# Kernel tuning notes

Hardware: AMD Instinct MI355X
Metric: run time of the kernel (lower is better)

## Reference

```python
import jax, jax.numpy as jnp
import numpy as np

DIM = 32          # image/vq dim (ImageTransform3D default dim=32 == vq.layers[0].dim)
CODEBOOK = 1024   # number of codebook entries
TOTAL = 4194304   # flat weight-vector length (multiple of DIM)


def setup_inputs() -> dict:
    key = jax.random.key(0)
    k1, k2, k3 = jax.random.split(key, 3)
    weights = jax.random.normal(k1, (TOTAL,), dtype=jnp.float32)
    condition = jax.random.normal(k2, (1, DIM, TOTAL // DIM), dtype=jnp.float32)
    codebook = jax.random.normal(k3, (CODEBOOK, DIM), dtype=jnp.float32)
    return {"weights": weights, "condition": condition, "codebook": codebook}


def reference(weights, condition, codebook):
    # --- ImageTransform3D.forward: pad flat weights to a multiple of DIM, view (1, DIM, -1)
    pad = (-weights.shape[0]) % DIM  # static
    if pad:
        weights = jnp.concatenate([weights, jnp.zeros((pad,), weights.dtype)])
    img = weights.reshape(1, DIM, -1)
    # --- TokenTransform3D: subtract condition, flatten to tokens of size DIM
    x = (img - condition).reshape(-1, DIM)  # [N, DIM]
    # --- VectorQuantize (freeze_codebook, eval): nearest-neighbour lookup
    d = (
        jnp.sum(x * x, axis=-1, keepdims=True)
        - 2.0 * (x @ codebook.T)
        + jnp.sum(codebook * codebook, axis=-1)
    )
    indices = jnp.argmin(d, axis=-1)  # [N] int32
    return indices
```

## Files before the change

kernel.cpp:

```cpp
#include <hip/hip_runtime.h>

#define TOTAL     4194304
#define DIM       32
#define NTOK      (TOTAL / DIM)
#define NCODE     1024
#define NCHUNK    8
#define CCODES    128
#define DELTA_EPS 2e-3f
#define FLAGBIT   0x40000000

typedef _Float16 half8   __attribute__((ext_vector_type(8)));
typedef float    floatx4 __attribute__((ext_vector_type(4)));

#define GLOAD_LDS16(g, l) \
    __builtin_amdgcn_global_load_lds((const __attribute__((address_space(1))) void*)(g), \
                                     (__attribute__((address_space(3))) void*)(l), 16, 0, 0)
#define GLOAD_LDS4(g, l) \
    __builtin_amdgcn_global_load_lds((const __attribute__((address_space(1))) void*)(g), \
                                     (__attribute__((address_space(3))) void*)(l), 4, 0, 0)

__global__ __launch_bounds__(64) void vq_prep(
    const float* __restrict__ cb, float* __restrict__ nhb,
    _Float16* __restrict__ Eh, _Float16* __restrict__ El)
{
    const int k = blockIdx.x * 64 + threadIdx.x;
    const float4* e4 = reinterpret_cast<const float4*>(cb) + (size_t)k * 8;
    float v[DIM];
    float4 t[8];
#pragma unroll
    for (int j = 0; j < 8; ++j) t[j] = e4[j];
#pragma unroll
    for (int j = 0; j < 8; ++j) {
        v[4 * j + 0] = t[j].x; v[4 * j + 1] = t[j].y;
        v[4 * j + 2] = t[j].z; v[4 * j + 3] = t[j].w;
    }
    float e2 = 0.0f;
#pragma unroll
    for (int i = 0; i < DIM; ++i) e2 = fmaf(v[i], v[i], e2);
    nhb[k] = -0.5f * e2;

    const int chunk = k >> 7, within = k & 127;
    const int step = within >> 4, l15 = within & 15;
#pragma unroll
    for (int l4 = 0; l4 < 4; ++l4) {
        half8 h, lo;
#pragma unroll
        for (int j = 0; j < 8; ++j) {
            float x = v[l4 * 8 + j];
            _Float16 hh = (_Float16)x;
            h[j]  = hh;
            lo[j] = (_Float16)(x - (float)hh);
        }
        const int slot = chunk * 512 + step * 64 + l4 * 16 + l15;
        *reinterpret_cast<half8*>(Eh + (size_t)slot * 8) = h;
        *reinterpret_cast<half8*>(El + (size_t)slot * 8) = lo;
    }
}

__global__ __launch_bounds__(256) void vq_main(
    const float* __restrict__ w, const float* __restrict__ c,
    const float* __restrict__ nhb, const _Float16* __restrict__ Eh,
    const _Float16* __restrict__ El, const float* __restrict__ cb,
    int* __restrict__ out)
{
    __shared__ _Float16 sEh[2][512 * 8];
    __shared__ _Float16 sEl[2][512 * 8];
    __shared__ float    snh[2][CCODES];
    __shared__ int      sOut[128];

    const int tid  = threadIdx.x;
    const int lane = tid & 63;
    const int wid  = tid >> 6;
    const int tok0 = blockIdx.x * 128 + wid * 32;
    const int l15  = lane & 15;
    const int l4   = lane >> 4;

    half8 xh[2], xl[2];
#pragma unroll
    for (int m = 0; m < 2; ++m) {
        const int token = tok0 + m * 16 + l15;
        const float4* pw = reinterpret_cast<const float4*>(w + (size_t)token * DIM + l4 * 8);
        const float4* pc = reinterpret_cast<const float4*>(c + (size_t)token * DIM + l4 * 8);
        float4 a0 = pw[0], a1 = pw[1], b0 = pc[0], b1 = pc[1];
        float xs[8] = {a0.x - b0.x, a0.y - b0.y, a0.z - b0.z, a0.w - b0.w,
                       a1.x - b1.x, a1.y - b1.y, a1.z - b1.z, a1.w - b1.w};
#pragma unroll
        for (int j = 0; j < 8; ++j) {
            _Float16 h = (_Float16)xs[j];
            xh[m][j] = h;
            xl[m][j] = (_Float16)(xs[j] - (float)h);
        }
    }

    const float NEGINF = __uint_as_float(0xFF800000u);
    float best[8], second[8];
#pragma unroll
    for (int q = 0; q < 8; ++q) { best[q] = NEGINF; second[q] = NEGINF; }

    auto stage = [&](int ch, int b) {
        const _Float16* gh = Eh + (size_t)ch * 4096;
        const _Float16* gl = El + (size_t)ch * 4096;
#pragma unroll
        for (int r2 = 0; r2 < 2; ++r2) {
            const int slot = r2 * 256 + wid * 64;
            GLOAD_LDS16(gh + (size_t)(slot + lane) * 8, &sEh[b][(size_t)slot * 8]);
            GLOAD_LDS16(gl + (size_t)(slot + lane) * 8, &sEl[b][(size_t)slot * 8]);
        }
        if (wid < 2) GLOAD_LDS4(nhb + ch * CCODES + wid * 64 + lane, &snh[b][wid * 64]);
    };

    stage(0, 0);
    __syncthreads();

    for (int ch = 0; ch < NCHUNK; ++ch) {
        const int b = ch & 1;
        if (ch < NCHUNK - 1) stage(ch + 1, b ^ 1);

#pragma unroll
        for (int sp = 0; sp < 4; ++sp) {
            const int sA = 2 * sp, sB = 2 * sp + 1;
            const half8 ehA = *reinterpret_cast<const half8*>(&sEh[b][(sA * 64 + lane) * 8]);
            const half8 elA = *reinterpret_cast<const half8*>(&sEl[b][(sA * 64 + lane) * 8]);
            const half8 ehB = *reinterpret_cast<const half8*>(&sEh[b][(sB * 64 + lane) * 8]);
            const half8 elB = *reinterpret_cast<const half8*>(&sEl[b][(sB * 64 + lane) * 8]);
            const float nhA = snh[b][sA * 16 + l15];
            const float nhB = snh[b][sB * 16 + l15];
            const unsigned ixA = 1023u - (unsigned)(ch * CCODES + sA * 16 + l15);
            const unsigned ixB = 1023u - (unsigned)(ch * CCODES + sB * 16 + l15);
            const floatx4 nA = {nhA, nhA, nhA, nhA};
            const floatx4 nB = {nhB, nhB, nhB, nhB};
#pragma unroll
            for (int m = 0; m < 2; ++m) {
                floatx4 aA = __builtin_amdgcn_mfma_f32_16x16x32_f16(xh[m], ehA, nA, 0, 0, 0);
                aA = __builtin_amdgcn_mfma_f32_16x16x32_f16(xl[m], ehA, aA, 0, 0, 0);
                aA = __builtin_amdgcn_mfma_f32_16x16x32_f16(xh[m], elA, aA, 0, 0, 0);
                floatx4 aB = __builtin_amdgcn_mfma_f32_16x16x32_f16(xh[m], ehB, nB, 0, 0, 0);
                aB = __builtin_amdgcn_mfma_f32_16x16x32_f16(xl[m], ehB, aB, 0, 0, 0);
                aB = __builtin_amdgcn_mfma_f32_16x16x32_f16(xh[m], elB, aB, 0, 0, 0);
#pragma unroll
                for (int r = 0; r < 4; ++r) {
                    const int q = m * 4 + r;
                    float pA = __uint_as_float((__float_as_uint(aA[r]) & 0xFFFFFC00u) | ixA);
                    float pB = __uint_as_float((__float_as_uint(aB[r]) & 0xFFFFFC00u) | ixB);
                    float t  = __builtin_amdgcn_fmed3f(pA, pB, best[q]);
                    second[q] = fmaxf(second[q], t);
                    best[q]   = fmaxf(fmaxf(best[q], pA), pB);
                }
            }
        }
        __syncthreads();
    }

#pragma unroll
    for (int sh = 1; sh < 16; sh <<= 1) {
#pragma unroll
        for (int q = 0; q < 8; ++q) {
            float bB = __shfl_xor(best[q], sh);
            float sB = __shfl_xor(second[q], sh);
            second[q] = fmaxf(fmaxf(second[q], sB), fminf(best[q], bB));
            best[q]   = fmaxf(best[q], bB);
        }
    }

    if (l15 == 0) {
#pragma unroll
        for (int m = 0; m < 2; ++m) {
#pragma unroll
            for (int r = 0; r < 4; ++r) {
                const int q = m * 4 + r;
                unsigned ub = __float_as_uint(best[q]);
                unsigned us = __float_as_uint(second[q]);
                float bv = __uint_as_float(ub & 0xFFFFFC00u);
                float sv = __uint_as_float(us & 0xFFFFFC00u);
                int eb = (int)((ub >> 23) & 255u);
                int es = (int)((us >> 23) & 255u);
                int em = eb > es ? eb : es;
                em = em > 12 ? em : 12;
                float thr = __uint_as_float((unsigned)(em - 11) << 23) + DELTA_EPS;
                int k = 1023 - (int)(ub & 1023u);
                sOut[wid * 32 + m * 16 + l4 * 4 + r] = ((bv - sv) < thr) ? (k | FLAGBIT) : k;
            }
        }
    }

    int myval = 0;
    if (lane < 32) myval = sOut[wid * 32 + lane];
    unsigned long long mask = __ballot(lane < 32 && (myval & FLAGBIT));
    while (mask) {
        const int src = __ffsll(mask) - 1;
        mask &= mask - 1;
        const int token = tok0 + src;

        float x[DIM];
#pragma unroll
        for (int i = 0; i < DIM; ++i) x[i] = w[(size_t)token * DIM + i] - c[(size_t)token * DIM + i];
        float x2 = 0.f;
#pragma unroll
        for (int i = 0; i < DIM; ++i) x2 = fmaf(x[i], x[i], x2);

        float dmin = INFINITY;
        int   kbest = 0;
#pragma unroll 2
        for (int i = 0; i < 16; ++i) {
            const int k = lane + 64 * i;
            const float* e = cb + (size_t)k * DIM;
            float dot = 0.f;
#pragma unroll
            for (int j = 0; j < DIM; ++j) dot = fmaf(x[j], e[j], dot);
            float e2 = -2.0f * nhb[k];
            float dd = fmaf(-2.0f, dot, x2) + e2;
            if (dd < dmin) { dmin = dd; kbest = k; }
        }
#pragma unroll
        for (int sh = 1; sh < 64; sh <<= 1) {
            float dB = __shfl_xor(dmin, sh);
            int   iB = __shfl_xor(kbest, sh);
            bool take = (dB < dmin) || (dB == dmin && iB < kbest);
            dmin = take ? dB : dmin;
            kbest = take ? iB : kbest;
        }
        if (lane == src) myval = kbest;
    }
    if (lane < 32) out[tok0 + lane] = myval;
}

extern "C" void kernel_launch(void* const* d_in, const int* in_sizes, int n_in,
                              void* d_out, int out_size, void* d_ws, size_t ws_size,
                              hipStream_t stream) {
    const float* w  = (const float*)d_in[0];
    const float* c  = (const float*)d_in[1];
    const float* cb = (const float*)d_in[2];
    int* out = (int*)d_out;

    char* wsb = (char*)d_ws;
    float*    nhb = (float*)wsb;
    _Float16* Eh  = (_Float16*)(wsb + 4096);
    _Float16* El  = (_Float16*)(wsb + 4096 + 65536);

    vq_prep<<<NCODE / 64, 64, 0, stream>>>(cb, nhb, Eh, El);
    vq_main<<<NTOK / 128, 256, 0, stream>>>(w, c, nhb, Eh, El, cb, out);
}
```

Measured before the change: 57.57 us.

## Double tokens per wave and stage codebook in two large single-buffered chunks

Each wave now handles 64 tokens instead of 32, so every codebook fragment read from LDS feeds four MFMA token tiles instead of two, and the grid is halved. The double-buffered 8-chunk pipeline becomes two 512-code chunks loaded synchronously, which removes per-chunk barriers but exposes the load latency. The top-2 update is simplified to one med3 and one max per candidate. Per-thread register use grows (16 best/second pairs, 4 token fragments) and LDS use rises to about 66KB, which may lower occupancy.

```diff
diff --git a/kernel.cpp b/kernel.cpp
--- a/kernel.cpp
+++ b/kernel.cpp
@@ -4,8 +4,7 @@
 #define DIM       32
 #define NTOK      (TOTAL / DIM)
 #define NCODE     1024
-#define NCHUNK    8
-#define CCODES    128
+#define CCODES    512
 #define DELTA_EPS 2e-3f
 #define FLAGBIT   0x40000000
 
@@ -39,7 +38,7 @@
     for (int i = 0; i < DIM; ++i) e2 = fmaf(v[i], v[i], e2);
     nhb[k] = -0.5f * e2;
 
-    const int chunk = k >> 7, within = k & 127;
+    const int chunk = k >> 9, within = k & 511;
     const int step = within >> 4, l15 = within & 15;
 #pragma unroll
     for (int l4 = 0; l4 < 4; ++l4) {
@@ -51,7 +50,7 @@
             h[j]  = hh;
             lo[j] = (_Float16)(x - (float)hh);
         }
-        const int slot = chunk * 512 + step * 64 + l4 * 16 + l15;
+        const int slot = chunk * 2048 + step * 64 + l4 * 16 + l15;
         *reinterpret_cast<half8*>(Eh + (size_t)slot * 8) = h;
         *reinterpret_cast<half8*>(El + (size_t)slot * 8) = lo;
     }
@@ -63,22 +62,22 @@
     const _Float16* __restrict__ El, const float* __restrict__ cb,
     int* __restrict__ out)
 {
-    __shared__ _Float16 sEh[2][512 * 8];
-    __shared__ _Float16 sEl[2][512 * 8];
-    __shared__ float    snh[2][CCODES];
-    __shared__ int      sOut[128];
+    __shared__ _Float16 sEh[2048 * 8];
+    __shared__ _Float16 sEl[2048 * 8];
+    __shared__ float    snh[CCODES];
+    __shared__ int      sOut[256];
 
     const int tid  = threadIdx.x;
     const int lane = tid & 63;
     const int wid  = tid >> 6;
-    const int tok0 = blockIdx.x * 128 + wid * 32;
+    const int tokw = blockIdx.x * 256 + wid * 64;
     const int l15  = lane & 15;
     const int l4   = lane >> 4;
 
-    half8 xh[2], xl[2];
-#pragma unroll
-    for (int m = 0; m < 2; ++m) {
-        const int token = tok0 + m * 16 + l15;
+    half8 xh[4], xl[4];
+#pragma unroll
+    for (int m = 0; m < 4; ++m) {
+        const int token = tokw + m * 16 + l15;
         const float4* pw = reinterpret_cast<const float4*>(w + (size_t)token * DIM + l4 * 8);
         const float4* pc = reinterpret_cast<const float4*>(c + (size_t)token * DIM + l4 * 8);
         float4 a0 = pw[0], a1 = pw[1], b0 = pc[0], b1 = pc[1];
@@ -93,68 +92,55 @@
     }
 
     const float NEGINF = __uint_as_float(0xFF800000u);
-    float best[8], second[8];
-#pragma unroll
-    for (int q = 0; q < 8; ++q) { best[q] = NEGINF; second[q] = NEGINF; }
-
-    auto stage = [&](int ch, int b) {
-        const _Float16* gh = Eh + (size_t)ch * 4096;
-        const _Float16* gl = El + (size_t)ch * 4096;
-#pragma unroll
-        for (int r2 = 0; r2 < 2; ++r2) {
-            const int slot = r2 * 256 + wid * 64;
-            GLOAD_LDS16(gh + (size_t)(slot + lane) * 8, &sEh[b][(size_t)slot * 8]);
-            GLOAD_LDS16(gl + (size_t)(slot + lane) * 8, &sEl[b][(size_t)slot * 8]);
-        }
-        if (wid < 2) GLOAD_LDS4(nhb + ch * CCODES + wid * 64 + lane, &snh[b][wid * 64]);
-    };
-
-    stage(0, 0);
-    __syncthreads();
-
-    for (int ch = 0; ch < NCHUNK; ++ch) {
-        const int b = ch & 1;
-        if (ch < NCHUNK - 1) stage(ch + 1, b ^ 1);
-
-#pragma unroll
-        for (int sp = 0; sp < 4; ++sp) {
-            const int sA = 2 * sp, sB = 2 * sp + 1;
-            const half8 ehA = *reinterpret_cast<const half8*>(&sEh[b][(sA * 64 + lane) * 8]);
-            const half8 elA = *reinterpret_cast<const half8*>(&sEl[b][(sA * 64 + lane) * 8]);
-            const half8 ehB = *reinterpret_cast<const half8*>(&sEh[b][(sB * 64 + lane) * 8]);
-            const half8 elB = *reinterpret_cast<const half8*>(&sEl[b][(sB * 64 + lane) * 8]);
-            const float nhA = snh[b][sA * 16 + l15];
-            const float nhB = snh[b][sB * 16 + l15];
-            const unsigned ixA = 1023u - (unsigned)(ch * CCODES + sA * 16 + l15);
-            const unsigned ixB = 1023u - (unsigned)(ch * CCODES + sB * 16 + l15);
-            const floatx4 nA = {nhA, nhA, nhA, nhA};
-            const floatx4 nB = {nhB, nhB, nhB, nhB};
-#pragma unroll
-            for (int m = 0; m < 2; ++m) {
-                floatx4 aA = __builtin_amdgcn_mfma_f32_16x16x32_f16(xh[m], ehA, nA, 0, 0, 0);
-                aA = __builtin_amdgcn_mfma_f32_16x16x32_f16(xl[m], ehA, aA, 0, 0, 0);
-                aA = __builtin_amdgcn_mfma_f32_16x16x32_f16(xh[m], elA, aA, 0, 0, 0);
-                floatx4 aB = __builtin_amdgcn_mfma_f32_16x16x32_f16(xh[m], ehB, nB, 0, 0, 0);
-                aB = __builtin_amdgcn_mfma_f32_16x16x32_f16(xl[m], ehB, aB, 0, 0, 0);
-                aB = __builtin_amdgcn_mfma_f32_16x16x32_f16(xh[m], elB, aB, 0, 0, 0);
+    float best[16], second[16];
+#pragma unroll
+    for (int q = 0; q < 16; ++q) { best[q] = NEGINF; second[q] = NEGINF; }
+
+    for (int ch = 0; ch < 2; ++ch) {
+        if (ch) __syncthreads();
+        {
+            const _Float16* gh = Eh + (size_t)ch * 16384;
+            const _Float16* gl = El + (size_t)ch * 16384;
+#pragma unroll
+            for (int r = 0; r < 8; ++r) {
+                const int slot = r * 256 + wid * 64;
+                GLOAD_LDS16(gh + (size_t)(slot + lane) * 8, sEh + (size_t)slot * 8);
+                GLOAD_LDS16(gl + (size_t)(slot + lane) * 8, sEl + (size_t)slot * 8);
+            }
+#pragma unroll
+            for (int r = 0; r < 2; ++r)
+                GLOAD_LDS4(nhb + ch * CCODES + wid * 128 + r * 64 + lane,
+                           snh + wid * 128 + r * 64);
+        }
+        __syncthreads();
+
+#pragma unroll 4
+        for (int step = 0; step < 32; ++step) {
+            const half8 eh = *reinterpret_cast<const half8*>(sEh + (size_t)(step * 64 + lane) * 8);
+            const half8 el = *reinterpret_cast<const half8*>(sEl + (size_t)(step * 64 + lane) * 8);
+            const float nh = snh[step * 16 + l15];
+            const unsigned ix = 1023u - (unsigned)(ch * CCODES + step * 16 + l15);
+            const floatx4 nv = {nh, nh, nh, nh};
+#pragma unroll
+            for (int m = 0; m < 4; ++m) {
+                floatx4 a = __builtin_amdgcn_mfma_f32_16x16x32_f16(xh[m], eh, nv, 0, 0, 0);
+                a = __builtin_amdgcn_mfma_f32_16x16x32_f16(xl[m], eh, a, 0, 0, 0);
+                a = __builtin_amdgcn_mfma_f32_16x16x32_f16(xh[m], el, a, 0, 0, 0);
 #pragma unroll
                 for (int r = 0; r < 4; ++r) {
                     const int q = m * 4 + r;
-                    float pA = __uint_as_float((__float_as_uint(aA[r]) & 0xFFFFFC00u) | ixA);
-                    float pB = __uint_as_float((__float_as_uint(aB[r]) & 0xFFFFFC00u) | ixB);
-                    float t  = __builtin_amdgcn_fmed3f(pA, pB, best[q]);
-                    second[q] = fmaxf(second[q], t);
-                    best[q]   = fmaxf(fmaxf(best[q], pA), pB);
+                    float p = __uint_as_float((__float_as_uint(a[r]) & 0xFFFFFC00u) | ix);
+                    second[q] = __builtin_amdgcn_fmed3f(p, best[q], second[q]);
+                    best[q]   = fmaxf(best[q], p);
                 }
             }
         }
-        __syncthreads();
     }
 
 #pragma unroll
     for (int sh = 1; sh < 16; sh <<= 1) {
 #pragma unroll
-        for (int q = 0; q < 8; ++q) {
+        for (int q = 0; q < 16; ++q) {
             float bB = __shfl_xor(best[q], sh);
             float sB = __shfl_xor(second[q], sh);
             second[q] = fmaxf(fmaxf(second[q], sB), fminf(best[q], bB));
@@ -164,7 +150,7 @@
 
     if (l15 == 0) {
 #pragma unroll
-        for (int m = 0; m < 2; ++m) {
+        for (int m = 0; m < 4; ++m) {
 #pragma unroll
             for (int r = 0; r < 4; ++r) {
                 const int q = m * 4 + r;
@@ -178,22 +164,22 @@
                 em = em > 12 ? em : 12;
                 float thr = __uint_as_float((unsigned)(em - 11) << 23) + DELTA_EPS;
                 int k = 1023 - (int)(ub & 1023u);
-                sOut[wid * 32 + m * 16 + l4 * 4 + r] = ((bv - sv) < thr) ? (k | FLAGBIT) : k;
+                sOut[wid * 64 + m * 16 + l4 * 4 + r] = ((bv - sv) < thr) ? (k | FLAGBIT) : k;
             }
         }
     }
 
-    int myval = 0;
-    if (lane < 32) myval = sOut[wid * 32 + lane];
-    unsigned long long mask = __ballot(lane < 32 && (myval & FLAGBIT));
+    int myval = sOut[wid * 64 + lane];
+    unsigned long long mask = __ballot((myval & FLAGBIT) != 0);
     while (mask) {
         const int src = __ffsll(mask) - 1;
         mask &= mask - 1;
-        const int token = tok0 + src;
+        const int token = tokw + src;
 
         float x[DIM];
 #pragma unroll
-        for (int i = 0; i < DIM; ++i) x[i] = w[(size_t)token * DIM + i] - c[(size_t)token * DIM + i];
+        for (int i = 0; i < DIM; ++i)
+            x[i] = w[(size_t)token * DIM + i] - c[(size_t)token * DIM + i];
         float x2 = 0.f;
 #pragma unroll
         for (int i = 0; i < DIM; ++i) x2 = fmaf(x[i], x[i], x2);
@@ -221,7 +207,8 @@
         }
         if (lane == src) myval = kbest;
     }
-    if (lane < 32) out[tok0 + lane] = myval;
+    out[tokw + lane] = myval;
+
 }
 
 extern "C" void kernel_launch(void* const* d_in, const int* in_sizes, int n_in,
@@ -238,5 +225,5 @@
     _Float16* El  = (_Float16*)(wsb + 4096 + 65536);
 
     vq_prep<<<NCODE / 64, 64, 0, stream>>>(cb, nhb, Eh, El);
-    vq_main<<<NTOK / 128, 256, 0, stream>>>(w, c, nhb, Eh, El, cb, out);
+    vq_main<<<NTOK / 256, 256, 0, stream>>>(w, c, nhb, Eh, El, cb, out);
 }
```

Measured after the change: 64.27 us. 11.6% more time.
